# Kernel tuning notes

Measured on AMD Instinct MI355X. Metric: run time of the kernel, lower is better.

## Reference

```python
import jax, jax.numpy as jnp
import numpy as np

N, E = 50000, 800000
F, H, M = 64, 128, 64  # feature_dim, hidden_dim, message_dim (message_dim must equal feature_dim)


def _mlp(x, W1, b1, W2, b2):
    return jnp.maximum(x @ W1 + b1, 0.0) @ W2 + b2


def setup_inputs() -> dict:
    key = jax.random.key(0)
    ks = jax.random.split(key, 20)
    p = lambda k, s: (jax.random.normal(k, s, jnp.float32) * 0.05)
    return {
        "z_h": jax.random.normal(ks[0], (N, F), jnp.float32),
        "pos_world": jax.random.normal(ks[1], (3,), jnp.float32),
        "edge_index": jax.random.randint(ks[2], (2, E), 0, N),
        "We1": p(ks[3], (2 * F + 8, H)), "be1": p(ks[4], (H,)),
        "We2": p(ks[5], (H, M)), "be2": p(ks[6], (M,)),
        "Wg1": p(ks[7], (2 * F + 8, H)), "bg1": p(ks[8], (H,)),
        "Wg2": p(ks[9], (H, 1)), "bg2": p(ks[10], (1,)),
        "Wn1": p(ks[11], (F + M, H)), "bn1": p(ks[12], (H,)),
        "Wn2": p(ks[13], (H, F)), "bn2": p(ks[14], (F,)),
        "Ww1": p(ks[15], (F + 3, H)), "bw1": p(ks[16], (H,)),
        "Ww2": p(ks[17], (H, M)), "bw2": p(ks[18], (M,)),
    }


def reference(z_h, pos_world, edge_index,
              We1, be1, We2, be2,
              Wg1, bg1, Wg2, bg2,
              Wn1, bn1, Wn2, bn2,
              Ww1, bw1, Ww2, bw2):
    src, tgt = edge_index[0], edge_index[1]
    zs = z_h[src]  # [E, F]
    zt = z_h[tgt]  # [E, F]

    # edge features: diff(3) + dist(1) + vel cross product(3) + its norm(1)
    diff = zs[:, 0:3] - zt[:, 0:3]
    dist = jnp.sum(diff * diff, axis=-1, keepdims=True)
    cross = jnp.cross(zs[:, 3:6], zt[:, 3:6])
    cross_n = jnp.linalg.norm(cross, axis=-1, keepdims=True)
    e_feat = jnp.concatenate([diff, dist, cross, cross_n], axis=-1)  # [E, 8]

    inp_edge = jnp.concatenate([zs, zt, e_feat], axis=-1)  # [E, 2F+8]
    m = _mlp(inp_edge, We1, be1, We2, be2)                 # [E, M]
    w = jax.nn.sigmoid(_mlp(inp_edge, Wg1, bg1, Wg2, bg2))  # [E, 1]

    # scatter_add weighted messages to target nodes
    m_agg_h = jax.ops.segment_sum(w * m, tgt, num_segments=N)  # [N, F] (M == F)

    # world message: sum over all nodes, broadcast back
    diff_world = z_h[:, 0:3] - pos_world
    inp_world = jnp.concatenate([z_h, diff_world], axis=-1)  # [N, F+3]
    m_h_w = _mlp(inp_world, Ww1, bw1, Ww2, bw2)              # [N, M]
    m_agg_w = jnp.sum(m_h_w, axis=0, keepdims=True)          # [1, M] -> broadcast

    m_agg_total = m_agg_h + m_agg_w
    inp_node = jnp.concatenate([z_h, m_agg_total], axis=-1)  # [N, F+M]
    delta_z_h = _mlp(inp_node, Wn1, bn1, Wn2, bn2)           # [N, F]
    return delta_z_h
```

## Files before the change

### kernel.cpp

```cpp
#include <hip/hip_runtime.h>
#include <math.h>

#define NN 50000
#define NE 800000
#define EBLOCKS (NE / 64)
#define WBLOCKS ((NN + 63) / 64)

typedef float     f32x4  __attribute__((ext_vector_type(4)));
typedef __bf16    bf16x8 __attribute__((ext_vector_type(8)));
typedef _Float16  f16x2  __attribute__((ext_vector_type(2)));
typedef _Float16  f16x8  __attribute__((ext_vector_type(8)));

#define WE1F_OFF 0
#define WE2F_OFF 5120
#define WN1F_OFF 6144
#define WN2F_OFF 8192
#define WW1F_OFF 9216
#define WW2F_OFF 10752
#define NCHUNKS  11776


__device__ inline bf16x8 pack8(float4 a, float4 b) {
    bf16x8 r;
    r[0] = (__bf16)a.x; r[1] = (__bf16)a.y; r[2] = (__bf16)a.z; r[3] = (__bf16)a.w;
    r[4] = (__bf16)b.x; r[5] = (__bf16)b.y; r[6] = (__bf16)b.z; r[7] = (__bf16)b.w;
    return r;
}

__device__ inline void pk_atomic_add_f16(void* addr, f16x2 v) {
#if __has_builtin(__builtin_amdgcn_global_atomic_fadd_v2f16)
    __builtin_amdgcn_global_atomic_fadd_v2f16((f16x2*)addr, v);
#else
    asm volatile("global_atomic_pk_add_f16 %0, %1, off"
                 :: "v"(addr), "v"(v) : "memory");
#endif
}

__global__ __launch_bounds__(512) void prep_z(
    const float* __restrict__ z, float* __restrict__ db)
{
    int i = blockIdx.x * 512 + threadIdx.x;
    if (i >= NN * 8) return;
    int node = i >> 3, c = i & 7;
    const float4* s = (const float4*)(z + (long)node * 64) + c * 2;
    float4 a = s[0], b = s[1];
    *(bf16x8*)((char*)db + (long)node * 256 + 128 + c * 16) = pack8(a, b);
}

__global__ __launch_bounds__(256) void pack_weights(
    const float* __restrict__ We1, const float* __restrict__ Wg1,
    const float* __restrict__ We2, const float* __restrict__ Wn1,
    const float* __restrict__ Wn2, const float* __restrict__ Ww1,
    const float* __restrict__ Ww2, bf16x8* __restrict__ wsF)
{
    int c = blockIdx.x * 256 + threadIdx.x;
    if (c >= NCHUNKS) return;
    const int lane = c & 63, l16 = lane & 15, row8 = ((lane >> 4) & 3) * 8;
    bf16x8 p;
    if (c < WE2F_OFF) {
        int ct = (c >> 6) & 15, kc = c >> 10;
        int col = ct * 16 + l16;
        const float* src = (col < 128) ? (We1 + col) : (Wg1 + (col - 128));
#pragma unroll
        for (int i = 0; i < 8; i++) {
            int r = kc * 32 + row8 + i;
            p[i] = (__bf16)((r < 136) ? src[(size_t)r * 128] : 0.f);
        }
    } else if (c < WN1F_OFF) {
        int cc = c - WE2F_OFF; int ct = (cc >> 6) & 3, kc = cc >> 8;
        int col = ct * 16 + l16;
#pragma unroll
        for (int i = 0; i < 8; i++)
            p[i] = (__bf16)We2[(size_t)(kc * 32 + row8 + i) * 64 + col];
    } else if (c < WN2F_OFF) {
        int cc = c - WN1F_OFF; int ct = (cc >> 6) & 7, kc = cc >> 9;
        int col = ct * 16 + l16;
#pragma unroll
        for (int i = 0; i < 8; i++)
            p[i] = (__bf16)Wn1[(size_t)(kc * 32 + row8 + i) * 128 + col];
    } else if (c < WW1F_OFF) {
        int cc = c - WN2F_OFF; int ct = (cc >> 6) & 3, kc = cc >> 8;
        int col = ct * 16 + l16;
#pragma unroll
        for (int i = 0; i < 8; i++)
            p[i] = (__bf16)Wn2[(size_t)(kc * 32 + row8 + i) * 64 + col];
    } else if (c < WW2F_OFF) {
        int cc = c - WW1F_OFF; int ct = (cc >> 6) & 7, kc = cc >> 9;
        int col = ct * 16 + l16;
#pragma unroll
        for (int i = 0; i < 8; i++) {
            int r = kc * 32 + row8 + i;
            p[i] = (__bf16)((r < 67) ? Ww1[(size_t)r * 128 + col] : 0.f);
        }
    } else {
        int cc = c - WW2F_OFF; int ct = (cc >> 6) & 3, kc = cc >> 8;
        int col = ct * 16 + l16;
#pragma unroll
        for (int i = 0; i < 8; i++)
            p[i] = (__bf16)Ww2[(size_t)(kc * 32 + row8 + i) * 64 + col];
    }
    wsF[c] = p;
}

union FusedLds {
    bf16x8 XF[1280];
    struct {
        bf16x8   HF[1024];
        _Float16 M[64 * 68];
    } s;
};

__global__ __launch_bounds__(512, 6) void fused_kernel(
    const float* __restrict__ z_h, const int* __restrict__ ei,
    const bf16x8* __restrict__ We1F, const bf16x8* __restrict__ We2F,
    const float* __restrict__ be1, const float* __restrict__ be2,
    const float* __restrict__ bg1, const float* __restrict__ Wg2,
    const float* __restrict__ bg2,
    const float* __restrict__ pos_world,
    const bf16x8* __restrict__ Ww1F, const bf16x8* __restrict__ Ww2F,
    const float* __restrict__ bw1, const float* __restrict__ bw2,
    float* __restrict__ magg_rows,
    float* __restrict__ m_agg_w)
{
    __shared__ FusedLds U;
    __shared__ int   tgt_s[64];
    __shared__ float gred[4][64];
    __shared__ float wgt[64];

    const int t = threadIdx.x;
    const int lane = t & 63, w = t >> 6;
    const int quad = lane >> 4, l16 = lane & 15;

    if (blockIdx.x >= EBLOCKS) {
        const int n0 = (blockIdx.x - EBLOCKS) * 64;
        {
            int nn = t >> 3, q = t & 7;
            int mt = nn >> 4, l16e = nn & 15;
            int node = n0 + nn; if (node >= NN) node = NN - 1;
            if (q < 4) {
                const float4* zr = (const float4*)(z_h + (long)node * 64) + q * 4;
                float4 a0 = zr[0], a1 = zr[1], a2 = zr[2], a3 = zr[3];
                int kcs = q >> 1, qa = (q & 1) * 2;
                U.XF[(kcs * 4 + mt) * 64 + qa * 16 + l16e]       = pack8(a0, a1);
                U.XF[(kcs * 4 + mt) * 64 + (qa + 1) * 16 + l16e] = pack8(a2, a3);
            } else if (q == 4) {
                float4 a0 = *(const float4*)(z_h + (long)node * 64);
                bf16x8 f;
#pragma unroll
                for (int i = 0; i < 8; i++) f[i] = (__bf16)0.f;
                f[0] = (__bf16)(a0.x - pos_world[0]);
                f[1] = (__bf16)(a0.y - pos_world[1]);
                f[2] = (__bf16)(a0.z - pos_world[2]);
                U.XF[(8 + mt) * 64 + l16e] = f;
            } else {
                bf16x8 z;
#pragma unroll
                for (int i = 0; i < 8; i++) z[i] = (__bf16)0.f;
                U.XF[(8 + mt) * 64 + (q - 4) * 16 + l16e] = z;
            }
        }
        __syncthreads();

        f32x4 acc[4];
        {
            float b = bw1[w * 16 + l16];
#pragma unroll
            for (int mt = 0; mt < 4; mt++) { f32x4 v = {b, b, b, b}; acc[mt] = v; }
        }
#pragma unroll
        for (int kc = 0; kc < 3; kc++) {
            bf16x8 bfr = Ww1F[(kc * 8 + w) * 64 + lane];
#pragma unroll
            for (int mt = 0; mt < 4; mt++)
                acc[mt] = __builtin_amdgcn_mfma_f32_16x16x32_bf16(
                    U.XF[(kc * 4 + mt) * 64 + lane], bfr, acc[mt], 0, 0, 0);
        }
        __syncthreads();

        {
            __bf16* HFp = (__bf16*)U.s.HF;
            int cw = w * 16 + l16;
            int kc2 = cw >> 5, quad2 = (cw >> 3) & 3, ii = cw & 7;
#pragma unroll
            for (int mt = 0; mt < 4; mt++)
#pragma unroll
                for (int r = 0; r < 4; r++)
                    HFp[(((kc2 * 4 + mt) * 64) + quad2 * 16 + quad * 4 + r) * 8 + ii] =
                        (__bf16)fmaxf(acc[mt][r], 0.f);
        }
        __syncthreads();

        {
            const int nt = w & 3, mh = w >> 2;
            f32x4 acc2[2];
            float b2 = bw2[nt * 16 + l16];
#pragma unroll
            for (int m = 0; m < 2; m++) { f32x4 v = {b2, b2, b2, b2}; acc2[m] = v; }
#pragma unroll
            for (int kc = 0; kc < 4; kc++) {
                bf16x8 b2f = Ww2F[(kc * 4 + nt) * 64 + lane];
#pragma unroll
                for (int m = 0; m < 2; m++)
                    acc2[m] = __builtin_amdgcn_mfma_f32_16x16x32_bf16(
                        U.s.HF[(kc * 4 + mh * 2 + m) * 64 + lane], b2f, acc2[m], 0, 0, 0);
            }
            float s = 0.f;
#pragma unroll
            for (int m = 0; m < 2; m++)
#pragma unroll
                for (int r = 0; r < 4; r++) {
                    int node = n0 + (mh * 2 + m) * 16 + quad * 4 + r;
                    s += (node < NN) ? acc2[m][r] : 0.f;
                }
            s += __shfl_xor(s, 16, 64);
            s += __shfl_xor(s, 32, 64);
            if (quad == 0) atomicAdd(m_agg_w + nt * 16 + l16, s);
        }
        return;
    }

    const int e0 = blockIdx.x * 64;

    {
        const int ee = t >> 3, q = t & 7;
        const int mt = ee >> 4, l16e = ee & 15;
        const int eg = e0 + ee;
        const int rs = ei[eg], rt = ei[NE + eg];
        const bf16x8* zs = (const bf16x8*)((const char*)magg_rows + (long)rs * 256 + 128);
        const bf16x8* zt = (const bf16x8*)((const char*)magg_rows + (long)rt * 256 + 128);
        bf16x8 sa = zs[q];
        bf16x8 ta = zt[q];
        const int kcs = q >> 2, qslot = q & 3;
        U.XF[(kcs * 4 + mt) * 64 + qslot * 16 + l16e]       = sa;
        U.XF[((kcs + 2) * 4 + mt) * 64 + qslot * 16 + l16e] = ta;
        if (q == 4) tgt_s[ee] = rt;
        if (q == 0) {
            float dx = (float)sa[0] - (float)ta[0];
            float dy = (float)sa[1] - (float)ta[1];
            float dz = (float)sa[2] - (float)ta[2];
            float ax = (float)sa[3], ay = (float)sa[4], az = (float)sa[5];
            float bx = (float)ta[3], by = (float)ta[4], bz = (float)ta[5];
            float cx = ay * bz - az * by;
            float cy = az * bx - ax * bz;
            float cz = ax * by - ay * bx;
            bf16x8 f;
            f[0] = (__bf16)dx; f[1] = (__bf16)dy; f[2] = (__bf16)dz;
            f[3] = (__bf16)(dx * dx + dy * dy + dz * dz);
            f[4] = (__bf16)cx; f[5] = (__bf16)cy; f[6] = (__bf16)cz;
            f[7] = (__bf16)sqrtf(cx * cx + cy * cy + cz * cz);
            U.XF[(16 + mt) * 64 + l16e] = f;
        } else if (q >= 5) {
            bf16x8 z;
#pragma unroll
            for (int i = 0; i < 8; i++) z[i] = (__bf16)0.f;
            U.XF[(16 + mt) * 64 + (q - 4) * 16 + l16e] = z;
        }
    }
    __syncthreads();

    f32x4 acc[4][2];
#pragma unroll
    for (int nt = 0; nt < 2; nt++) {
        int col = (w * 2 + nt) * 16 + l16;
        float b = (col < 128) ? be1[col] : bg1[col - 128];
#pragma unroll
        for (int mt = 0; mt < 4; mt++) { f32x4 v = {b, b, b, b}; acc[mt][nt] = v; }
    }
    bf16x8 bcur0 = We1F[(w * 2) * 64 + lane];
    bf16x8 bcur1 = We1F[(w * 2 + 1) * 64 + lane];
#pragma unroll
    for (int kc = 0; kc < 5; kc++) {
        bf16x8 bnx0, bnx1;
        if (kc < 4) {
            bnx0 = We1F[((kc + 1) * 16 + w * 2) * 64 + lane];
            bnx1 = We1F[((kc + 1) * 16 + w * 2 + 1) * 64 + lane];
        }
#pragma unroll
        for (int mt = 0; mt < 4; mt++) {
            bf16x8 af = U.XF[(kc * 4 + mt) * 64 + lane];
            acc[mt][0] = __builtin_amdgcn_mfma_f32_16x16x32_bf16(af, bcur0, acc[mt][0], 0, 0, 0);
            acc[mt][1] = __builtin_amdgcn_mfma_f32_16x16x32_bf16(af, bcur1, acc[mt][1], 0, 0, 0);
        }
        bcur0 = bnx0; bcur1 = bnx1;
    }
    __syncthreads();

    if (w < 4) {
        __bf16* HFp = (__bf16*)U.s.HF;
#pragma unroll
        for (int nt = 0; nt < 2; nt++) {
            int cw = (w * 2 + nt) * 16 + l16;
            int kc2 = cw >> 5, quad2 = (cw >> 3) & 3, ii = cw & 7;
#pragma unroll
            for (int mt = 0; mt < 4; mt++)
#pragma unroll
                for (int r = 0; r < 4; r++)
                    HFp[(((kc2 * 4 + mt) * 64) + quad2 * 16 + quad * 4 + r) * 8 + ii] =
                        (__bf16)fmaxf(acc[mt][nt][r], 0.f);
        }
    } else {
        float gp[4][4];
#pragma unroll
        for (int mt = 0; mt < 4; mt++)
#pragma unroll
            for (int r = 0; r < 4; r++) gp[mt][r] = 0.f;
#pragma unroll
        for (int nt = 0; nt < 2; nt++) {
            float wg = Wg2[((w - 4) * 2 + nt) * 16 + l16];
#pragma unroll
            for (int mt = 0; mt < 4; mt++)
#pragma unroll
                for (int r = 0; r < 4; r++)
                    gp[mt][r] += fmaxf(acc[mt][nt][r], 0.f) * wg;
        }
#pragma unroll
        for (int mask = 1; mask < 16; mask <<= 1)
#pragma unroll
            for (int mt = 0; mt < 4; mt++)
#pragma unroll
                for (int r = 0; r < 4; r++)
                    gp[mt][r] += __shfl_xor(gp[mt][r], mask, 64);
        if (l16 == 0) {
#pragma unroll
            for (int mt = 0; mt < 4; mt++)
#pragma unroll
                for (int r = 0; r < 4; r++)
                    gred[(w - 4) & 3][mt * 16 + quad * 4 + r] = gp[mt][r];
        }
    }
    __syncthreads();

    if (t < 64) {
        float g = bg2[0] + gred[0][t] + gred[1][t] + gred[2][t] + gred[3][t];
        wgt[t] = 1.f / (1.f + __expf(-g));
    }

    f32x4 acc2[4];
    if (w < 4) {
        float b2 = be2[w * 16 + l16];
#pragma unroll
        for (int mt = 0; mt < 4; mt++) { f32x4 v = {b2, b2, b2, b2}; acc2[mt] = v; }
        bf16x8 c2 = We2F[w * 64 + lane];
#pragma unroll
        for (int kc = 0; kc < 4; kc++) {
            bf16x8 n2;
            if (kc < 3) n2 = We2F[((kc + 1) * 4 + w) * 64 + lane];
#pragma unroll
            for (int mt = 0; mt < 4; mt++)
                acc2[mt] = __builtin_amdgcn_mfma_f32_16x16x32_bf16(
                    U.s.HF[(kc * 4 + mt) * 64 + lane], c2, acc2[mt], 0, 0, 0);
            c2 = n2;
        }
    }
    __syncthreads();

    if (w < 4) {
#pragma unroll
        for (int mt = 0; mt < 4; mt++)
#pragma unroll
            for (int r = 0; r < 4; r++) {
                int edge = mt * 16 + quad * 4 + r;
                U.s.M[edge * 68 + w * 16 + l16] =
                    (_Float16)(acc2[mt][r] * wgt[edge]);
            }
    }
    __syncthreads();

    {
        const int p = t & 31, eb = t >> 5;
        char* base = (char*)magg_rows;
#pragma unroll
        for (int k = 0; k < 4; k++) {
            int e = eb + k * 16;
            f16x2 v = *(const f16x2*)&U.s.M[e * 68 + p * 2];
            pk_atomic_add_f16(base + (long)tgt_s[e] * 256 + p * 4, v);
        }
    }
}

__global__ __launch_bounds__(512, 4) void node_kernel(
    const float* __restrict__ m_agg_w,
    const bf16x8* __restrict__ Wn1F, const bf16x8* __restrict__ Wn2F,
    const float* __restrict__ bn1, const float* __restrict__ bn2,
    float* __restrict__ outp)
{
    __shared__ union { bf16x8 XF[1024]; bf16x8 HF[1024]; } U;
    const int t = threadIdx.x;
    const int n0 = blockIdx.x * 64;
    const int lane = t & 63, w = t >> 6;
    const int quad = lane >> 4, l16 = lane & 15;

    {
        int nn = t >> 3, q = t & 7;
        int mt = nn >> 4, l16e = nn & 15;
        int node = n0 + nn; if (node >= NN) node = NN - 1;
        int half = q >> 2, sub = q & 3;
        bf16x8 c0, c1;
        if (half == 0) {
            const bf16x8* zr = (const bf16x8*)((const char*)outp + (long)node * 256 + 128) + sub * 2;
            c0 = zr[0]; c1 = zr[1];
        } else {
            const f16x8* mr = (const f16x8*)((const char*)outp + (long)node * 256) + sub * 2;
            f16x8 r0 = mr[0], r1 = mr[1];
            const float* mw = m_agg_w + sub * 16;
#pragma unroll
            for (int i = 0; i < 8; i++) {
                c0[i] = (__bf16)((float)r0[i] + mw[i]);
                c1[i] = (__bf16)((float)r1[i] + mw[i + 8]);
            }
        }
        int kcs = (sub >> 1) + half * 2, qa = (sub & 1) * 2;
        U.XF[(kcs * 4 + mt) * 64 + qa * 16 + l16e]       = c0;
        U.XF[(kcs * 4 + mt) * 64 + (qa + 1) * 16 + l16e] = c1;
    }
    __syncthreads();

    f32x4 acc[4];
    {
        float b = bn1[w * 16 + l16];
#pragma unroll
        for (int mt = 0; mt < 4; mt++) { f32x4 v = {b, b, b, b}; acc[mt] = v; }
    }
#pragma unroll
    for (int kc = 0; kc < 4; kc++) {
        bf16x8 bfr = Wn1F[(kc * 8 + w) * 64 + lane];
#pragma unroll
        for (int mt = 0; mt < 4; mt++)
            acc[mt] = __builtin_amdgcn_mfma_f32_16x16x32_bf16(
                U.XF[(kc * 4 + mt) * 64 + lane], bfr, acc[mt], 0, 0, 0);
    }
    __syncthreads();

    {
        __bf16* HFp = (__bf16*)U.HF;
        int cw = w * 16 + l16;
        int kc2 = cw >> 5, quad2 = (cw >> 3) & 3, ii = cw & 7;
#pragma unroll
        for (int mt = 0; mt < 4; mt++)
#pragma unroll
            for (int r = 0; r < 4; r++)
                HFp[(((kc2 * 4 + mt) * 64) + quad2 * 16 + quad * 4 + r) * 8 + ii] =
                    (__bf16)fmaxf(acc[mt][r], 0.f);
    }
    __syncthreads();

    {
        const int nt = w & 3, mh = w >> 2;
        f32x4 acc2[2];
        float b2 = bn2[nt * 16 + l16];
#pragma unroll
        for (int m = 0; m < 2; m++) { f32x4 v = {b2, b2, b2, b2}; acc2[m] = v; }
#pragma unroll
        for (int kc = 0; kc < 4; kc++) {
            bf16x8 b2f = Wn2F[(kc * 4 + nt) * 64 + lane];
#pragma unroll
            for (int m = 0; m < 2; m++)
                acc2[m] = __builtin_amdgcn_mfma_f32_16x16x32_bf16(
                    U.HF[(kc * 4 + mh * 2 + m) * 64 + lane], b2f, acc2[m], 0, 0, 0);
        }
#pragma unroll
        for (int m = 0; m < 2; m++)
#pragma unroll
            for (int r = 0; r < 4; r++) {
                int node = n0 + (mh * 2 + m) * 16 + quad * 4 + r;
                if (node < NN)
                    outp[(long)node * 64 + nt * 16 + l16] = acc2[m][r];
            }
    }
}

extern "C" void kernel_launch(void* const* d_in, const int* in_sizes, int n_in,
                              void* d_out, int out_size, void* d_ws, size_t ws_size,
                              hipStream_t stream)
{
    const float* z_h       = (const float*)d_in[0];
    const float* pos_world = (const float*)d_in[1];
    const int*   ei        = (const int*)d_in[2];
    const float* We1 = (const float*)d_in[3];  const float* be1 = (const float*)d_in[4];
    const float* We2 = (const float*)d_in[5];  const float* be2 = (const float*)d_in[6];
    const float* Wg1 = (const float*)d_in[7];  const float* bg1 = (const float*)d_in[8];
    const float* Wg2 = (const float*)d_in[9];  const float* bg2 = (const float*)d_in[10];
    const float* Wn1 = (const float*)d_in[11]; const float* bn1 = (const float*)d_in[12];
    const float* Wn2 = (const float*)d_in[13]; const float* bn2 = (const float*)d_in[14];
    const float* Ww1 = (const float*)d_in[15]; const float* bw1 = (const float*)d_in[16];
    const float* Ww2 = (const float*)d_in[17]; const float* bw2 = (const float*)d_in[18];

    float*  outp    = (float*)d_out;
    float*  m_agg_w = (float*)d_ws;
    bf16x8* wsF     = (bf16x8*)((char*)d_ws + 256);

    hipMemsetAsync(d_out, 0, (size_t)NN * 64 * sizeof(float), stream);
    hipMemsetAsync(d_ws, 0, 256, stream);

    prep_z<<<(NN * 8 + 511) / 512, 512, 0, stream>>>(z_h, outp);
    pack_weights<<<(NCHUNKS + 255) / 256, 256, 0, stream>>>(
        We1, Wg1, We2, Wn1, Wn2, Ww1, Ww2, wsF);
    fused_kernel<<<EBLOCKS + WBLOCKS, 512, 0, stream>>>(
        z_h, ei, wsF + WE1F_OFF, wsF + WE2F_OFF,
        be1, be2, bg1, Wg2, bg2,
        pos_world, wsF + WW1F_OFF, wsF + WW2F_OFF, bw1, bw2,
        outp, m_agg_w);
    node_kernel<<<(NN + 63) / 64, 512, 0, stream>>>(
        m_agg_w, wsF + WN1F_OFF, wsF + WN2F_OFF, bn1, bn2, outp);
}
```

Before: 294.4 us.

## Restructure edge kernel so each wave owns 32 edges with register-resident inputs

```diff
diff --git a/kernel.cpp b/kernel.cpp
--- a/kernel.cpp
+++ b/kernel.cpp
@@ -3,11 +3,13 @@
 
 #define NN 50000
 #define NE 800000
-#define EBLOCKS (NE / 64)
+#define EBW 128
+#define EBLOCKS (NE / EBW)
 #define WBLOCKS ((NN + 63) / 64)
 
 typedef float     f32x4  __attribute__((ext_vector_type(4)));
 typedef __bf16    bf16x8 __attribute__((ext_vector_type(8)));
+typedef __bf16    bf16x4 __attribute__((ext_vector_type(4)));
 typedef _Float16  f16x2  __attribute__((ext_vector_type(2)));
 typedef _Float16  f16x8  __attribute__((ext_vector_type(8)));
 
@@ -45,6 +47,8 @@
     const float4* s = (const float4*)(z + (long)node * 64) + c * 2;
     float4 a = s[0], b = s[1];
     *(bf16x8*)((char*)db + (long)node * 256 + 128 + c * 16) = pack8(a, b);
+    float4 zz = {0.f, 0.f, 0.f, 0.f};
+    *(float4*)((char*)db + (long)node * 256 + c * 16) = zz;
 }
 
 __global__ __launch_bounds__(256) void pack_weights(
@@ -103,14 +107,11 @@
 }
 
 union FusedLds {
-    bf16x8 XF[1280];
-    struct {
-        bf16x8   HF[1024];
-        _Float16 M[64 * 68];
-    } s;
+    struct { char HM[4][8192]; int tgt[4][32]; } e;
+    bf16x8 XF[1024];
 };
 
-__global__ __launch_bounds__(512, 6) void fused_kernel(
+__global__ __launch_bounds__(256, 4) void fused_kernel(
     const float* __restrict__ z_h, const int* __restrict__ ei,
     const bf16x8* __restrict__ We1F, const bf16x8* __restrict__ We2F,
     const float* __restrict__ be1, const float* __restrict__ be2,
@@ -123,10 +124,6 @@
     float* __restrict__ m_agg_w)
 {
     __shared__ FusedLds U;
-    __shared__ int   tgt_s[64];
-    __shared__ float gred[4][64];
-    __shared__ float wgt[64];
-
     const int t = threadIdx.x;
     const int lane = t & 63, w = t >> 6;
     const int quad = lane >> 4, l16 = lane & 15;
@@ -134,17 +131,15 @@
     if (blockIdx.x >= EBLOCKS) {
         const int n0 = (blockIdx.x - EBLOCKS) * 64;
         {
-            int nn = t >> 3, q = t & 7;
+            int nn = t >> 2, q = t & 3;
             int mt = nn >> 4, l16e = nn & 15;
             int node = n0 + nn; if (node >= NN) node = NN - 1;
-            if (q < 4) {
-                const float4* zr = (const float4*)(z_h + (long)node * 64) + q * 4;
-                float4 a0 = zr[0], a1 = zr[1], a2 = zr[2], a3 = zr[3];
-                int kcs = q >> 1, qa = (q & 1) * 2;
-                U.XF[(kcs * 4 + mt) * 64 + qa * 16 + l16e]       = pack8(a0, a1);
-                U.XF[(kcs * 4 + mt) * 64 + (qa + 1) * 16 + l16e] = pack8(a2, a3);
-            } else if (q == 4) {
-                float4 a0 = *(const float4*)(z_h + (long)node * 64);
+            const float4* zr = (const float4*)(z_h + (long)node * 64) + q * 4;
+            float4 a0 = zr[0], a1 = zr[1], a2 = zr[2], a3 = zr[3];
+            int kcs = q >> 1, qa = (q & 1) * 2;
+            U.XF[(kcs * 4 + mt) * 64 + qa * 16 + l16e]       = pack8(a0, a1);
+            U.XF[(kcs * 4 + mt) * 64 + (qa + 1) * 16 + l16e] = pack8(a2, a3);
+            if (q == 0) {
                 bf16x8 f;
 #pragma unroll
                 for (int i = 0; i < 8; i++) f[i] = (__bf16)0.f;
@@ -153,227 +148,227 @@
                 f[2] = (__bf16)(a0.z - pos_world[2]);
                 U.XF[(8 + mt) * 64 + l16e] = f;
             } else {
-                bf16x8 z;
-#pragma unroll
-                for (int i = 0; i < 8; i++) z[i] = (__bf16)0.f;
-                U.XF[(8 + mt) * 64 + (q - 4) * 16 + l16e] = z;
+                bf16x8 z8;
+#pragma unroll
+                for (int i = 0; i < 8; i++) z8[i] = (__bf16)0.f;
+                U.XF[(8 + mt) * 64 + q * 16 + l16e] = z8;
             }
         }
         __syncthreads();
 
-        f32x4 acc[4];
+        f32x4 acc[4][2];
+#pragma unroll
+        for (int nt2 = 0; nt2 < 2; nt2++) {
+            float b = bw1[(w * 2 + nt2) * 16 + l16];
+#pragma unroll
+            for (int mt = 0; mt < 4; mt++) { f32x4 v = {b, b, b, b}; acc[mt][nt2] = v; }
+        }
+#pragma unroll
+        for (int kc = 0; kc < 3; kc++) {
+#pragma unroll
+            for (int nt2 = 0; nt2 < 2; nt2++) {
+                bf16x8 bfr = Ww1F[(kc * 8 + w * 2 + nt2) * 64 + lane];
+#pragma unroll
+                for (int mt = 0; mt < 4; mt++)
+                    acc[mt][nt2] = __builtin_amdgcn_mfma_f32_16x16x32_bf16(
+                        U.XF[(kc * 4 + mt) * 64 + lane], bfr, acc[mt][nt2], 0, 0, 0);
+            }
+        }
+        __syncthreads();
+
         {
-            float b = bw1[w * 16 + l16];
-#pragma unroll
-            for (int mt = 0; mt < 4; mt++) { f32x4 v = {b, b, b, b}; acc[mt] = v; }
-        }
-#pragma unroll
-        for (int kc = 0; kc < 3; kc++) {
-            bf16x8 bfr = Ww1F[(kc * 8 + w) * 64 + lane];
-#pragma unroll
-            for (int mt = 0; mt < 4; mt++)
-                acc[mt] = __builtin_amdgcn_mfma_f32_16x16x32_bf16(
-                    U.XF[(kc * 4 + mt) * 64 + lane], bfr, acc[mt], 0, 0, 0);
+            __bf16* HFp = (__bf16*)U.XF;
+#pragma unroll
+            for (int nt2 = 0; nt2 < 2; nt2++) {
+                int cw = (w * 2 + nt2) * 16 + l16;
+                int kc2 = cw >> 5, quad2 = (cw >> 3) & 3, ii = cw & 7;
+#pragma unroll
+                for (int mt = 0; mt < 4; mt++)
+#pragma unroll
+                    for (int r = 0; r < 4; r++)
+                        HFp[(((kc2 * 4 + mt) * 64) + quad2 * 16 + quad * 4 + r) * 8 + ii] =
+                            (__bf16)fmaxf(acc[mt][nt2][r], 0.f);
+            }
         }
         __syncthreads();
 
         {
-            __bf16* HFp = (__bf16*)U.s.HF;
-            int cw = w * 16 + l16;
-            int kc2 = cw >> 5, quad2 = (cw >> 3) & 3, ii = cw & 7;
-#pragma unroll
-            for (int mt = 0; mt < 4; mt++)
-#pragma unroll
-                for (int r = 0; r < 4; r++)
-                    HFp[(((kc2 * 4 + mt) * 64) + quad2 * 16 + quad * 4 + r) * 8 + ii] =
-                        (__bf16)fmaxf(acc[mt][r], 0.f);
-        }
-        __syncthreads();
-
-        {
-            const int nt = w & 3, mh = w >> 2;
-            f32x4 acc2[2];
-            float b2 = bw2[nt * 16 + l16];
-#pragma unroll
-            for (int m = 0; m < 2; m++) { f32x4 v = {b2, b2, b2, b2}; acc2[m] = v; }
+            f32x4 acc2[2][2];
+            float b2 = bw2[w * 16 + l16];
+#pragma unroll
+            for (int mh = 0; mh < 2; mh++)
+#pragma unroll
+                for (int m = 0; m < 2; m++) { f32x4 v = {b2, b2, b2, b2}; acc2[mh][m] = v; }
 #pragma unroll
             for (int kc = 0; kc < 4; kc++) {
-                bf16x8 b2f = Ww2F[(kc * 4 + nt) * 64 + lane];
+                bf16x8 b2f = Ww2F[(kc * 4 + w) * 64 + lane];
+#pragma unroll
+                for (int mh = 0; mh < 2; mh++)
+#pragma unroll
+                    for (int m = 0; m < 2; m++)
+                        acc2[mh][m] = __builtin_amdgcn_mfma_f32_16x16x32_bf16(
+                            U.XF[(kc * 4 + mh * 2 + m) * 64 + lane], b2f, acc2[mh][m], 0, 0, 0);
+            }
+            float s = 0.f;
+#pragma unroll
+            for (int mh = 0; mh < 2; mh++)
 #pragma unroll
                 for (int m = 0; m < 2; m++)
-                    acc2[m] = __builtin_amdgcn_mfma_f32_16x16x32_bf16(
-                        U.s.HF[(kc * 4 + mh * 2 + m) * 64 + lane], b2f, acc2[m], 0, 0, 0);
-            }
-            float s = 0.f;
-#pragma unroll
-            for (int m = 0; m < 2; m++)
-#pragma unroll
-                for (int r = 0; r < 4; r++) {
-                    int node = n0 + (mh * 2 + m) * 16 + quad * 4 + r;
-                    s += (node < NN) ? acc2[m][r] : 0.f;
-                }
+#pragma unroll
+                    for (int r = 0; r < 4; r++) {
+                        int node = n0 + (mh * 2 + m) * 16 + quad * 4 + r;
+                        s += (node < NN) ? acc2[mh][m][r] : 0.f;
+                    }
             s += __shfl_xor(s, 16, 64);
             s += __shfl_xor(s, 32, 64);
-            if (quad == 0) atomicAdd(m_agg_w + nt * 16 + l16, s);
+            if (quad == 0) atomicAdd(m_agg_w + w * 16 + l16, s);
         }
         return;
     }
 
-    const int e0 = blockIdx.x * 64;
-
-    {
-        const int ee = t >> 3, q = t & 7;
-        const int mt = ee >> 4, l16e = ee & 15;
-        const int eg = e0 + ee;
-        const int rs = ei[eg], rt = ei[NE + eg];
-        const bf16x8* zs = (const bf16x8*)((const char*)magg_rows + (long)rs * 256 + 128);
-        const bf16x8* zt = (const bf16x8*)((const char*)magg_rows + (long)rt * 256 + 128);
-        bf16x8 sa = zs[q];
-        bf16x8 ta = zt[q];
-        const int kcs = q >> 2, qslot = q & 3;
-        U.XF[(kcs * 4 + mt) * 64 + qslot * 16 + l16e]       = sa;
-        U.XF[((kcs + 2) * 4 + mt) * 64 + qslot * 16 + l16e] = ta;
-        if (q == 4) tgt_s[ee] = rt;
-        if (q == 0) {
-            float dx = (float)sa[0] - (float)ta[0];
-            float dy = (float)sa[1] - (float)ta[1];
-            float dz = (float)sa[2] - (float)ta[2];
-            float ax = (float)sa[3], ay = (float)sa[4], az = (float)sa[5];
-            float bx = (float)ta[3], by = (float)ta[4], bz = (float)ta[5];
+    const int e0 = blockIdx.x * EBW + w * 32;
+    char* HMw = U.e.HM[w];
+
+    bf16x8 x[2][5];
+#pragma unroll
+    for (int nt = 0; nt < 2; nt++) {
+        int eg = e0 + nt * 16 + l16;
+        int rs = ei[eg], rt = ei[NE + eg];
+        if (quad == 0) U.e.tgt[w][nt * 16 + l16] = rt;
+        const char* zs = (const char*)magg_rows + (long)rs * 256 + 128;
+        const char* zt = (const char*)magg_rows + (long)rt * 256 + 128;
+        bf16x8 s0 = *(const bf16x8*)(zs + quad * 16);
+        bf16x8 s1 = *(const bf16x8*)(zs + 64 + quad * 16);
+        bf16x8 t0 = *(const bf16x8*)(zt + quad * 16);
+        bf16x8 t1 = *(const bf16x8*)(zt + 64 + quad * 16);
+        x[nt][0] = s0; x[nt][1] = s1; x[nt][2] = t0; x[nt][3] = t1;
+        bf16x8 f;
+#pragma unroll
+        for (int i = 0; i < 8; i++) f[i] = (__bf16)0.f;
+        if (quad == 0) {
+            float dx = (float)s0[0] - (float)t0[0];
+            float dy = (float)s0[1] - (float)t0[1];
+            float dz = (float)s0[2] - (float)t0[2];
+            float ax = (float)s0[3], ay = (float)s0[4], az = (float)s0[5];
+            float bx = (float)t0[3], by = (float)t0[4], bz = (float)t0[5];
             float cx = ay * bz - az * by;
             float cy = az * bx - ax * bz;
             float cz = ax * by - ay * bx;
-            bf16x8 f;
             f[0] = (__bf16)dx; f[1] = (__bf16)dy; f[2] = (__bf16)dz;
             f[3] = (__bf16)(dx * dx + dy * dy + dz * dz);
             f[4] = (__bf16)cx; f[5] = (__bf16)cy; f[6] = (__bf16)cz;
             f[7] = (__bf16)sqrtf(cx * cx + cy * cy + cz * cz);
-            U.XF[(16 + mt) * 64 + l16e] = f;
-        } else if (q >= 5) {
-            bf16x8 z;
-#pragma unroll
-            for (int i = 0; i < 8; i++) z[i] = (__bf16)0.f;
-            U.XF[(16 + mt) * 64 + (q - 4) * 16 + l16e] = z;
-        }
-    }
-    __syncthreads();
-
-    f32x4 acc[4][2];
+        }
+        x[nt][4] = f;
+    }
+
+    float gpv[2] = {0.f, 0.f};
+#pragma unroll
+    for (int p = 0; p < 4; p++) {
+        f32x4 a[4][2];
+#pragma unroll
+        for (int mi = 0; mi < 4; mi++) {
+            const float* bp = (p < 2) ? (be1 + (p * 4 + mi) * 16)
+                                      : (bg1 + ((p - 2) * 4 + mi) * 16);
+            float4 b4 = *(const float4*)(bp + quad * 4);
+            f32x4 v; v[0] = b4.x; v[1] = b4.y; v[2] = b4.z; v[3] = b4.w;
+            a[mi][0] = v; a[mi][1] = v;
+        }
+#pragma unroll
+        for (int kc = 0; kc < 5; kc++)
+#pragma unroll
+            for (int mi = 0; mi < 4; mi++) {
+                bf16x8 fr = We1F[(kc * 16 + p * 4 + mi) * 64 + lane];
+                a[mi][0] = __builtin_amdgcn_mfma_f32_16x16x32_bf16(fr, x[0][kc], a[mi][0], 0, 0, 0);
+                a[mi][1] = __builtin_amdgcn_mfma_f32_16x16x32_bf16(fr, x[1][kc], a[mi][1], 0, 0, 0);
+            }
+        if (p < 2) {
+#pragma unroll
+            for (int mi = 0; mi < 4; mi++)
+#pragma unroll
+                for (int nt = 0; nt < 2; nt++) {
+                    bf16x4 hv;
+#pragma unroll
+                    for (int r = 0; r < 4; r++)
+                        hv[r] = (__bf16)fmaxf(a[mi][nt][r], 0.f);
+                    int mt = p * 4 + mi;
+                    int chunk = mt * 2 + (quad >> 1);
+                    *(bf16x4*)(HMw + nt * 4096 + chunk * 256 + l16 * 16 + (quad & 1) * 8) = hv;
+                }
+        } else {
+#pragma unroll
+            for (int mi = 0; mi < 4; mi++) {
+                float4 wg = *(const float4*)(Wg2 + ((p - 2) * 4 + mi) * 16 + quad * 4);
+#pragma unroll
+                for (int nt = 0; nt < 2; nt++) {
+                    gpv[nt] += fmaxf(a[mi][nt][0], 0.f) * wg.x;
+                    gpv[nt] += fmaxf(a[mi][nt][1], 0.f) * wg.y;
+                    gpv[nt] += fmaxf(a[mi][nt][2], 0.f) * wg.z;
+                    gpv[nt] += fmaxf(a[mi][nt][3], 0.f) * wg.w;
+                }
+            }
+        }
+    }
+
+    float wgt[2];
+    {
+        float b2g = bg2[0];
+#pragma unroll
+        for (int nt = 0; nt < 2; nt++) {
+            float g = gpv[nt];
+            g += __shfl_xor(g, 16, 64);
+            g += __shfl_xor(g, 32, 64);
+            wgt[nt] = 1.f / (1.f + __expf(-(g + b2g)));
+        }
+    }
+
+    f32x4 c2[4][2];
+#pragma unroll
+    for (int mct = 0; mct < 4; mct++) {
+        float4 b4 = *(const float4*)(be2 + mct * 16 + quad * 4);
+        f32x4 v; v[0] = b4.x; v[1] = b4.y; v[2] = b4.z; v[3] = b4.w;
+        c2[mct][0] = v; c2[mct][1] = v;
+    }
+#pragma unroll
+    for (int kc = 0; kc < 4; kc++) {
+        bf16x8 h0 = *(const bf16x8*)(HMw + 0 * 4096 + (kc * 4 + quad) * 256 + l16 * 16);
+        bf16x8 h1 = *(const bf16x8*)(HMw + 1 * 4096 + (kc * 4 + quad) * 256 + l16 * 16);
+#pragma unroll
+        for (int mct = 0; mct < 4; mct++) {
+            bf16x8 wf = We2F[(kc * 4 + mct) * 64 + lane];
+            c2[mct][0] = __builtin_amdgcn_mfma_f32_16x16x32_bf16(wf, h0, c2[mct][0], 0, 0, 0);
+            c2[mct][1] = __builtin_amdgcn_mfma_f32_16x16x32_bf16(wf, h1, c2[mct][1], 0, 0, 0);
+        }
+    }
+
 #pragma unroll
     for (int nt = 0; nt < 2; nt++) {
-        int col = (w * 2 + nt) * 16 + l16;
-        float b = (col < 128) ? be1[col] : bg1[col - 128];
-#pragma unroll
-        for (int mt = 0; mt < 4; mt++) { f32x4 v = {b, b, b, b}; acc[mt][nt] = v; }
-    }
-    bf16x8 bcur0 = We1F[(w * 2) * 64 + lane];
-    bf16x8 bcur1 = We1F[(w * 2 + 1) * 64 + lane];
-#pragma unroll
-    for (int kc = 0; kc < 5; kc++) {
-        bf16x8 bnx0, bnx1;
-        if (kc < 4) {
-            bnx0 = We1F[((kc + 1) * 16 + w * 2) * 64 + lane];
-            bnx1 = We1F[((kc + 1) * 16 + w * 2 + 1) * 64 + lane];
-        }
-#pragma unroll
-        for (int mt = 0; mt < 4; mt++) {
-            bf16x8 af = U.XF[(kc * 4 + mt) * 64 + lane];
-            acc[mt][0] = __builtin_amdgcn_mfma_f32_16x16x32_bf16(af, bcur0, acc[mt][0], 0, 0, 0);
-            acc[mt][1] = __builtin_amdgcn_mfma_f32_16x16x32_bf16(af, bcur1, acc[mt][1], 0, 0, 0);
-        }
-        bcur0 = bnx0; bcur1 = bnx1;
-    }
-    __syncthreads();
-
-    if (w < 4) {
-        __bf16* HFp = (__bf16*)U.s.HF;
+        char* Mw = HMw + nt * 4096;
+#pragma unroll
+        for (int mct = 0; mct < 4; mct++) {
+            f16x2 v0, v1;
+            v0[0] = (_Float16)(c2[mct][nt][0] * wgt[nt]);
+            v0[1] = (_Float16)(c2[mct][nt][1] * wgt[nt]);
+            v1[0] = (_Float16)(c2[mct][nt][2] * wgt[nt]);
+            v1[1] = (_Float16)(c2[mct][nt][3] * wgt[nt]);
+            *(f16x2*)(Mw + l16 * 132 + (mct * 16 + quad * 4) * 2)     = v0;
+            *(f16x2*)(Mw + l16 * 132 + (mct * 16 + quad * 4) * 2 + 4) = v1;
+        }
+    }
+
+    {
+        const int pp = lane & 31, eh = lane >> 5;
+        char* base = (char*)magg_rows;
 #pragma unroll
         for (int nt = 0; nt < 2; nt++) {
-            int cw = (w * 2 + nt) * 16 + l16;
-            int kc2 = cw >> 5, quad2 = (cw >> 3) & 3, ii = cw & 7;
-#pragma unroll
-            for (int mt = 0; mt < 4; mt++)
-#pragma unroll
-                for (int r = 0; r < 4; r++)
-                    HFp[(((kc2 * 4 + mt) * 64) + quad2 * 16 + quad * 4 + r) * 8 + ii] =
-                        (__bf16)fmaxf(acc[mt][nt][r], 0.f);
-        }
-    } else {
-        float gp[4][4];
-#pragma unroll
-        for (int mt = 0; mt < 4; mt++)
-#pragma unroll
-            for (int r = 0; r < 4; r++) gp[mt][r] = 0.f;
-#pragma unroll
-        for (int nt = 0; nt < 2; nt++) {
-            float wg = Wg2[((w - 4) * 2 + nt) * 16 + l16];
-#pragma unroll
-            for (int mt = 0; mt < 4; mt++)
-#pragma unroll
-                for (int r = 0; r < 4; r++)
-                    gp[mt][r] += fmaxf(acc[mt][nt][r], 0.f) * wg;
-        }
-#pragma unroll
-        for (int mask = 1; mask < 16; mask <<= 1)
-#pragma unroll
-            for (int mt = 0; mt < 4; mt++)
-#pragma unroll
-                for (int r = 0; r < 4; r++)
-                    gp[mt][r] += __shfl_xor(gp[mt][r], mask, 64);
-        if (l16 == 0) {
-#pragma unroll
-            for (int mt = 0; mt < 4; mt++)
-#pragma unroll
-                for (int r = 0; r < 4; r++)
-                    gred[(w - 4) & 3][mt * 16 + quad * 4 + r] = gp[mt][r];
-        }
-    }
-    __syncthreads();
-
-    if (t < 64) {
-        float g = bg2[0] + gred[0][t] + gred[1][t] + gred[2][t] + gred[3][t];
-        wgt[t] = 1.f / (1.f + __expf(-g));
-    }
-
-    f32x4 acc2[4];
-    if (w < 4) {
-        float b2 = be2[w * 16 + l16];
-#pragma unroll
-        for (int mt = 0; mt < 4; mt++) { f32x4 v = {b2, b2, b2, b2}; acc2[mt] = v; }
-        bf16x8 c2 = We2F[w * 64 + lane];
-#pragma unroll
-        for (int kc = 0; kc < 4; kc++) {
-            bf16x8 n2;
-            if (kc < 3) n2 = We2F[((kc + 1) * 4 + w) * 64 + lane];
-#pragma unroll
-            for (int mt = 0; mt < 4; mt++)
-                acc2[mt] = __builtin_amdgcn_mfma_f32_16x16x32_bf16(
-                    U.s.HF[(kc * 4 + mt) * 64 + lane], c2, acc2[mt], 0, 0, 0);
-            c2 = n2;
-        }
-    }
-    __syncthreads();
-
-    if (w < 4) {
-#pragma unroll
-        for (int mt = 0; mt < 4; mt++)
-#pragma unroll
-            for (int r = 0; r < 4; r++) {
-                int edge = mt * 16 + quad * 4 + r;
-                U.s.M[edge * 68 + w * 16 + l16] =
-                    (_Float16)(acc2[mt][r] * wgt[edge]);
-            }
-    }
-    __syncthreads();
-
-    {
-        const int p = t & 31, eb = t >> 5;
-        char* base = (char*)magg_rows;
-#pragma unroll
-        for (int k = 0; k < 4; k++) {
-            int e = eb + k * 16;
-            f16x2 v = *(const f16x2*)&U.s.M[e * 68 + p * 2];
-            pk_atomic_add_f16(base + (long)tgt_s[e] * 256 + p * 4, v);
+            char* Mw = HMw + nt * 4096;
+#pragma unroll
+            for (int k = 0; k < 8; k++) {
+                int e = eh + k * 2;
+                f16x2 v = *(const f16x2*)(Mw + e * 132 + pp * 4);
+                int trow = U.e.tgt[w][nt * 16 + e];
+                pk_atomic_add_f16(base + (long)trow * 256 + pp * 4, v);
+            }
         }
     }
 }
@@ -489,13 +484,12 @@
     float*  m_agg_w = (float*)d_ws;
     bf16x8* wsF     = (bf16x8*)((char*)d_ws + 256);
 
-    hipMemsetAsync(d_out, 0, (size_t)NN * 64 * sizeof(float), stream);
     hipMemsetAsync(d_ws, 0, 256, stream);
 
     prep_z<<<(NN * 8 + 511) / 512, 512, 0, stream>>>(z_h, outp);
     pack_weights<<<(NCHUNKS + 255) / 256, 256, 0, stream>>>(
         We1, Wg1, We2, Wn1, Wn2, Ww1, Ww2, wsF);
-    fused_kernel<<<EBLOCKS + WBLOCKS, 512, 0, stream>>>(
+    fused_kernel<<<EBLOCKS + WBLOCKS, 256, 0, stream>>>(
         z_h, ei, wsF + WE1F_OFF, wsF + WE2F_OFF,
         be1, be2, bg1, Wg2, bg2,
         pos_world, wsF + WW1F_OFF, wsF + WW2F_OFF, bw1, bw2,
```

After: 332.8 us. +13.1%, slower.

## Fuse memsets and prep kernels; compute gate via shuffles; split node LDS buffers

Applied to the files above, without the earlier changes.

```diff
diff --git a/kernel.cpp b/kernel.cpp
--- a/kernel.cpp
+++ b/kernel.cpp
@@ -36,24 +36,27 @@
 #endif
 }
 
-__global__ __launch_bounds__(512) void prep_z(
-    const float* __restrict__ z, float* __restrict__ db)
-{
-    int i = blockIdx.x * 512 + threadIdx.x;
-    if (i >= NN * 8) return;
-    int node = i >> 3, c = i & 7;
-    const float4* s = (const float4*)(z + (long)node * 64) + c * 2;
-    float4 a = s[0], b = s[1];
-    *(bf16x8*)((char*)db + (long)node * 256 + 128 + c * 16) = pack8(a, b);
-}
-
-__global__ __launch_bounds__(256) void pack_weights(
+__global__ __launch_bounds__(256) void prep(
     const float* __restrict__ We1, const float* __restrict__ Wg1,
     const float* __restrict__ We2, const float* __restrict__ Wn1,
     const float* __restrict__ Wn2, const float* __restrict__ Ww1,
-    const float* __restrict__ Ww2, bf16x8* __restrict__ wsF)
+    const float* __restrict__ Ww2, bf16x8* __restrict__ wsF,
+    const float* __restrict__ z, float* __restrict__ db,
+    float* __restrict__ m_agg_w)
 {
-    int c = blockIdx.x * 256 + threadIdx.x;
+    const int c = blockIdx.x * 256 + threadIdx.x;
+
+    if (c < 64) m_agg_w[c] = 0.f;
+
+    if (c < NN * 8) {
+        int node = c >> 3, q = c & 7;
+        const float4* s = (const float4*)(z + (long)node * 64) + q * 2;
+        float4 a = s[0], b = s[1];
+        *(bf16x8*)((char*)db + (long)node * 256 + 128 + q * 16) = pack8(a, b);
+        float4 zz = {0.f, 0.f, 0.f, 0.f};
+        *(float4*)((char*)db + (long)node * 256 + q * 16) = zz;
+    }
+
     if (c >= NCHUNKS) return;
     const int lane = c & 63, l16 = lane & 15, row8 = ((lane >> 4) & 3) * 8;
     bf16x8 p;
@@ -125,7 +128,6 @@
     __shared__ FusedLds U;
     __shared__ int   tgt_s[64];
     __shared__ float gred[4][64];
-    __shared__ float wgt[64];
 
     const int t = threadIdx.x;
     const int lane = t & 63, w = t >> 6;
@@ -330,13 +332,8 @@
     }
     __syncthreads();
 
-    if (t < 64) {
-        float g = bg2[0] + gred[0][t] + gred[1][t] + gred[2][t] + gred[3][t];
-        wgt[t] = 1.f / (1.f + __expf(-g));
-    }
-
-    f32x4 acc2[4];
     if (w < 4) {
+        f32x4 acc2[4];
         float b2 = be2[w * 16 + l16];
 #pragma unroll
         for (int mt = 0; mt < 4; mt++) { f32x4 v = {b2, b2, b2, b2}; acc2[mt] = v; }
@@ -351,17 +348,22 @@
                     U.s.HF[(kc * 4 + mt) * 64 + lane], c2, acc2[mt], 0, 0, 0);
             c2 = n2;
         }
-    }
-    __syncthreads();
-
-    if (w < 4) {
+
+        float wgtreg;
+        {
+            float g = bg2[0] + gred[0][lane] + gred[1][lane]
+                             + gred[2][lane] + gred[3][lane];
+            wgtreg = 1.f / (1.f + __expf(-g));
+        }
+
 #pragma unroll
         for (int mt = 0; mt < 4; mt++)
 #pragma unroll
             for (int r = 0; r < 4; r++) {
                 int edge = mt * 16 + quad * 4 + r;
+                float wg = __shfl(wgtreg, edge, 64);
                 U.s.M[edge * 68 + w * 16 + l16] =
-                    (_Float16)(acc2[mt][r] * wgt[edge]);
+                    (_Float16)(acc2[mt][r] * wg);
             }
     }
     __syncthreads();
@@ -384,7 +386,8 @@
     const float* __restrict__ bn1, const float* __restrict__ bn2,
     float* __restrict__ outp)
 {
-    __shared__ union { bf16x8 XF[1024]; bf16x8 HF[1024]; } U;
+    __shared__ bf16x8 XF[1024];
+    __shared__ bf16x8 HF[1024];
     const int t = threadIdx.x;
     const int n0 = blockIdx.x * 64;
     const int lane = t & 63, w = t >> 6;
@@ -410,8 +413,8 @@
             }
         }
         int kcs = (sub >> 1) + half * 2, qa = (sub & 1) * 2;
-        U.XF[(kcs * 4 + mt) * 64 + qa * 16 + l16e]       = c0;
-        U.XF[(kcs * 4 + mt) * 64 + (qa + 1) * 16 + l16e] = c1;
+        XF[(kcs * 4 + mt) * 64 + qa * 16 + l16e]       = c0;
+        XF[(kcs * 4 + mt) * 64 + (qa + 1) * 16 + l16e] = c1;
     }
     __syncthreads();
 
@@ -427,12 +430,11 @@
 #pragma unroll
         for (int mt = 0; mt < 4; mt++)
             acc[mt] = __builtin_amdgcn_mfma_f32_16x16x32_bf16(
-                U.XF[(kc * 4 + mt) * 64 + lane], bfr, acc[mt], 0, 0, 0);
-    }
-    __syncthreads();
+                XF[(kc * 4 + mt) * 64 + lane], bfr, acc[mt], 0, 0, 0);
+    }
 
     {
-        __bf16* HFp = (__bf16*)U.HF;
+        __bf16* HFp = (__bf16*)HF;
         int cw = w * 16 + l16;
         int kc2 = cw >> 5, quad2 = (cw >> 3) & 3, ii = cw & 7;
 #pragma unroll
@@ -456,7 +458,7 @@
 #pragma unroll
             for (int m = 0; m < 2; m++)
                 acc2[m] = __builtin_amdgcn_mfma_f32_16x16x32_bf16(
-                    U.HF[(kc * 4 + mh * 2 + m) * 64 + lane], b2f, acc2[m], 0, 0, 0);
+                    HF[(kc * 4 + mh * 2 + m) * 64 + lane], b2f, acc2[m], 0, 0, 0);
         }
 #pragma unroll
         for (int m = 0; m < 2; m++)
@@ -489,12 +491,8 @@
     float*  m_agg_w = (float*)d_ws;
     bf16x8* wsF     = (bf16x8*)((char*)d_ws + 256);
 
-    hipMemsetAsync(d_out, 0, (size_t)NN * 64 * sizeof(float), stream);
-    hipMemsetAsync(d_ws, 0, 256, stream);
-
-    prep_z<<<(NN * 8 + 511) / 512, 512, 0, stream>>>(z_h, outp);
-    pack_weights<<<(NCHUNKS + 255) / 256, 256, 0, stream>>>(
-        We1, Wg1, We2, Wn1, Wn2, Ww1, Ww2, wsF);
+    prep<<<(NN * 8 + 255) / 256, 256, 0, stream>>>(
+        We1, Wg1, We2, Wn1, Wn2, Ww1, Ww2, wsF, z_h, outp, m_agg_w);
     fused_kernel<<<EBLOCKS + WBLOCKS, 512, 0, stream>>>(
         z_h, ei, wsF + WE1F_OFF, wsF + WE2F_OFF,
         be1, be2, bg1, Wg2, bg2,
```

New measurement: 287.8 us. -2.2%, faster.
